# Kernel optimization log

Hardware: AMD Instinct MI355X
Metric: run time of the kernel (lower is better)

Reference implementation:

```python
import jax, jax.numpy as jnp
import numpy as np

B, N = 16, 4096
IOU_THR = 0.7
SCORE_THR = 0.5
MAX_PROPS = 300
IMG = 800.0


def setup_inputs() -> dict:
    key = jax.random.key(0)
    k1, k2, k3 = jax.random.split(key, 3)
    xy = jax.random.uniform(k1, (B, N, 2), dtype=jnp.float32) * IMG
    wh = jax.random.uniform(k2, (B, N, 2), dtype=jnp.float32) * 192.0 + 8.0
    proposals = jnp.concatenate([xy, xy + wh], axis=-1)  # [B,N,4] valid x1y1x2y2
    cls_scores = jax.random.uniform(k3, (B, N, 2), dtype=jnp.float32)
    return {"proposals": proposals, "cls_scores": cls_scores}


def _nms_indices(boxes, scores):
    """Greedy NMS on one image. Returns MAX_PROPS indices into boxes (padded
    with the last kept index, matching the torch module's padding)."""
    boxes = jax.lax.stop_gradient(boxes)
    scores = jax.lax.stop_gradient(scores)
    n = boxes.shape[0]
    valid = scores > SCORE_THR
    # Sort descending; invalid boxes pushed to the end and pre-suppressed.
    order = jnp.argsort(-jnp.where(valid, scores, -jnp.inf))
    b = boxes[order]
    v = valid[order]
    x1, y1, x2, y2 = b[:, 0], b[:, 1], b[:, 2], b[:, 3]
    area = (x2 - x1) * (y2 - y1)
    idxs = jnp.arange(n)

    def body(i, suppressed):
        keep_i = jnp.logical_not(suppressed[i])
        xi1 = jnp.maximum(x1[i], x1)
        yi1 = jnp.maximum(y1[i], y1)
        xi2 = jnp.minimum(x2[i], x2)
        yi2 = jnp.minimum(y2[i], y2)
        inter = jnp.clip(xi2 - xi1, 0.0) * jnp.clip(yi2 - yi1, 0.0)
        iou = inter / (area[i] + area - inter)
        # torch keeps ious < thr, i.e. suppresses iou >= thr among later boxes
        return suppressed | (keep_i & (iou >= IOU_THR) & (idxs > i))

    suppressed = jax.lax.fori_loop(0, n, body, jnp.logical_not(v))
    keep = jnp.logical_not(suppressed)
    # Kept positions (in sorted/greedy order) first, then sentinel n.
    pos = jnp.sort(jnp.where(keep, idxs, n))
    nk = keep.sum()
    slot = jnp.minimum(jnp.arange(MAX_PROPS), jnp.maximum(nk - 1, 0))
    sel_sorted = jnp.clip(pos[slot], 0, n - 1)  # clip guards nk==0
    return order[sel_sorted]  # [MAX_PROPS] indices into original boxes


def reference(proposals, cls_scores):
    scores = cls_scores[..., 1]  # [B,N]
    sel = jax.vmap(_nms_indices)(proposals, scores)  # [B,MAX_PROPS]
    out_boxes = jnp.take_along_axis(proposals, sel[..., None], axis=1)  # [B,MAX_PROPS,4]
    out_scores = jnp.take_along_axis(scores, sel, axis=1)  # [B,MAX_PROPS]
    return out_boxes, out_scores
```

## Files before the change

kernel.cpp:

```cpp
#include <hip/hip_runtime.h>

typedef unsigned long long ull;

#define BB 16
#define NN 4096
#define NT 1024
#define EPT 4
#define MAXP 300
#define IOU_THRESH 0.7f
#define SCORE_THR 0.5f

#define FNT 512
#define FEPT (NN / FNT)
#define CCAP 1024
#define RTOP 512
#define RW (RTOP / 64)

__device__ __forceinline__ bool iou_ge(float ix1, float iy1, float ix2, float iy2, float ia,
                                       float x1, float y1, float x2, float y2, float aj) {
    float xx1 = fmaxf(ix1, x1);
    float yy1 = fmaxf(iy1, y1);
    float xx2 = fminf(ix2, x2);
    float yy2 = fminf(iy2, y2);
    float iw = fmaxf(__fsub_rn(xx2, xx1), 0.0f);
    float ih = fmaxf(__fsub_rn(yy2, yy1), 0.0f);
    float inter = __fmul_rn(iw, ih);
    float uni = __fsub_rn(__fadd_rn(ia, aj), inter);
    float iou = __fdiv_rn(inter, uni);
    return iou >= IOU_THRESH;
}

__global__ __launch_bounds__(FNT, 1) void filter_sort_kernel(const float* __restrict__ proposals,
                                                             const float* __restrict__ cls,
                                                             float* __restrict__ wx1, float* __restrict__ wy1,
                                                             float* __restrict__ wx2, float* __restrict__ wy2,
                                                             float* __restrict__ war,
                                                             unsigned* __restrict__ cidx,
                                                             unsigned* __restrict__ wnv,
                                                             unsigned* __restrict__ need0) {
    __shared__ ull ck[CCAP];
    __shared__ unsigned hist[256];
    __shared__ unsigned swsum[FNT / 64];
    __shared__ unsigned s_nv, s_t, s_abv, s_sz;

    const int b = blockIdx.x, tid = threadIdx.x;
    const unsigned lane = tid & 63, wv = tid >> 6;
    const float* Cb = cls + (size_t)b * NN * 2;
    const float4* Pb4 = (const float4*)(proposals + (size_t)b * NN * 4);

    if (tid < 256) hist[tid] = 0;
    ck[tid] = 0; ck[tid + FNT] = 0;
    if (tid == 0) s_nv = 0;
    __syncthreads();

    unsigned lv = 0;
    #pragma unroll
    for (int c = 0; c < FEPT; ++c) {
        int i = c * FNT + tid;
        float sc = Cb[2 * i + 1];
        if (sc > SCORE_THR) {
            unsigned mb = __float_as_uint(sc) | 0x80000000u;
            atomicAdd(&hist[mb >> 24], 1u);
            ++lv;
        }
    }
    for (int off = 32; off > 0; off >>= 1) lv += __shfl_down(lv, off, 64);
    if (lane == 0) atomicAdd(&s_nv, lv);
    __syncthreads();

    const unsigned nv = s_nv;
    const unsigned target = nv < (unsigned)RTOP ? nv : (unsigned)RTOP;

    if (tid < 64) {
        unsigned h[4], S[4], local = 0;
        #pragma unroll
        for (int c = 0; c < 4; ++c) { h[c] = hist[tid * 4 + c]; local += h[c]; }
        unsigned inc = local;
        for (int off = 1; off < 64; off <<= 1) {
            unsigned t = __shfl_down(inc, off, 64);
            if (tid + off < 64) inc += t;
        }
        unsigned above = inc - local;
        S[3] = above + h[3];
        S[2] = S[3] + h[2];
        S[1] = S[2] + h[1];
        S[0] = S[1] + h[0];
        int bestc = -1;
        #pragma unroll
        for (int c = 3; c >= 0; --c) if (bestc < 0 && S[c] >= target) bestc = c;
        ull m = __ballot(bestc >= 0);
        int L = 63 - __builtin_clzll(m);
        if (tid == L) {
            s_t = (unsigned)(tid * 4 + bestc);
            s_abv = S[bestc] - h[bestc];
            s_sz = h[bestc];
        }
    }
    __syncthreads();
    const unsigned t1 = s_t;
    const unsigned abv1 = s_abv;
    const int lvl2 = (s_abv + s_sz > CCAP);
    unsigned t2 = 0, Ccand;

    if (lvl2) {
        if (tid < 256) hist[tid] = 0;
        __syncthreads();
        #pragma unroll
        for (int c = 0; c < FEPT; ++c) {
            int i = c * FNT + tid;
            float sc = Cb[2 * i + 1];
            if (sc > SCORE_THR) {
                unsigned mb = __float_as_uint(sc) | 0x80000000u;
                if ((mb >> 24) == t1) atomicAdd(&hist[(mb >> 16) & 0xFFu], 1u);
            }
        }
        __syncthreads();
        const unsigned target2 = target - abv1;
        if (tid < 64) {
            unsigned h[4], S[4], local = 0;
            #pragma unroll
            for (int c = 0; c < 4; ++c) { h[c] = hist[tid * 4 + c]; local += h[c]; }
            unsigned inc = local;
            for (int off = 1; off < 64; off <<= 1) {
                unsigned t = __shfl_down(inc, off, 64);
                if (tid + off < 64) inc += t;
            }
            unsigned above = inc - local;
            S[3] = above + h[3];
            S[2] = S[3] + h[2];
            S[1] = S[2] + h[1];
            S[0] = S[1] + h[0];
            int bestc = -1;
            #pragma unroll
            for (int c = 3; c >= 0; --c) if (bestc < 0 && S[c] >= target2) bestc = c;
            ull m = __ballot(bestc >= 0);
            int L = 63 - __builtin_clzll(m);
            if (tid == L) {
                s_t = (unsigned)(tid * 4 + bestc);
                s_abv = S[bestc] - h[bestc];
                s_sz = h[bestc];
            }
        }
        __syncthreads();
        t2 = s_t;
        Ccand = abv1 + s_abv + s_sz;
    } else {
        Ccand = s_abv + s_sz;
    }

    if (tid == 0) { need0[b] = (Ccand > CCAP) ? 1u : 0u; wnv[b] = nv; }

    unsigned pf[FEPT];
    ull keys[FEPT];
    unsigned lc = 0;
    #pragma unroll
    for (int c = 0; c < FEPT; ++c) {
        int i = c * FNT + tid;
        float sc = Cb[2 * i + 1];
        unsigned p = 0; ull key = 0;
        if (sc > SCORE_THR) {
            unsigned mb = __float_as_uint(sc) | 0x80000000u;
            unsigned b1 = mb >> 24;
            if (b1 > t1 || (b1 == t1 && (!lvl2 || ((mb >> 16) & 0xFFu) >= t2))) {
                p = 1;
                key = ((ull)mb << 32) | (unsigned)(~i);
            }
        }
        pf[c] = p; keys[c] = key; lc += p;
    }
    unsigned inc = lc;
    for (int off = 1; off < 64; off <<= 1) {
        unsigned o = __shfl_up(inc, off, 64);
        if (lane >= (unsigned)off) inc += o;
    }
    if (lane == 63) swsum[wv] = inc;
    __syncthreads();
    if (tid == 0) {
        unsigned run = 0;
        for (int w = 0; w < FNT / 64; ++w) { unsigned t = swsum[w]; swsum[w] = run; run += t; }
    }
    __syncthreads();
    unsigned pos = swsum[wv] + (inc - lc);
    #pragma unroll
    for (int c = 0; c < FEPT; ++c) {
        if (pf[c]) {
            if (pos < CCAP) ck[pos] = keys[c];
            ++pos;
        }
    }
    __syncthreads();

    for (unsigned k = 2; k <= CCAP; k <<= 1) {
        for (unsigned j = k >> 1; j > 0; j >>= 1) {
            unsigned p = tid;
            unsigned low = p & (j - 1);
            unsigned i2 = ((p ^ low) << 1) | low;
            unsigned ixj = i2 | j;
            ull a = ck[i2], c2 = ck[ixj];
            if ((a < c2) == ((i2 & k) == 0)) { ck[i2] = c2; ck[ixj] = a; }
            __syncthreads();
        }
    }

    if (tid < RTOP) {
        const size_t base = (size_t)b * RTOP;
        ull key = ck[tid];
        unsigned oi = key ? ~(unsigned)key : 0u;
        float4 v = make_float4(0.f, 0.f, 0.f, 0.f);
        if (key) v = Pb4[oi];
        wx1[base + tid] = v.x; wy1[base + tid] = v.y;
        wx2[base + tid] = v.z; wy2[base + tid] = v.w;
        war[base + tid] = __fmul_rn(__fsub_rn(v.z, v.x), __fsub_rn(v.w, v.y));
        cidx[base + tid] = oi;
    }
}

__global__ __launch_bounds__(256) void mask512_kernel(const float* __restrict__ wx1, const float* __restrict__ wy1,
                                                      const float* __restrict__ wx2, const float* __restrict__ wy2,
                                                      const float* __restrict__ war,
                                                      const unsigned* __restrict__ wnv,
                                                      ull* __restrict__ m8) {
    __shared__ float sx1[RTOP], sy1[RTOP], sx2[RTOP], sy2[RTOP], sar[RTOP];
    const int img = blockIdx.y;
    const unsigned nv = wnv[img];
    const unsigned R2 = nv < (unsigned)RTOP ? nv : (unsigned)RTOP;
    if (R2 == 0) return;
    const int tid = threadIdx.x;
    const size_t base = (size_t)img * RTOP;

    for (int idx = tid; idx < RTOP; idx += 256) {
        sx1[idx] = wx1[base + idx];
        sy1[idx] = wy1[base + idx];
        sx2[idx] = wx2[base + idx];
        sy2[idx] = wy2[base + idx];
        sar[idx] = war[base + idx];
    }
    __syncthreads();

    const unsigned lane = tid & 63;
    const unsigned wvimg = blockIdx.x * 4 + (tid >> 6);
    const unsigned wlastR = (R2 - 1) >> 6;
    ull* mimg = m8 + base * RW;

    for (unsigned i = wvimg; i < R2; i += 32) {
        float ix1 = sx1[i], iy1 = sy1[i], ix2 = sx2[i], iy2 = sy2[i], ia = sar[i];
        const unsigned w0 = i >> 6;
        ull my = 0;
        for (unsigned w = w0; w <= wlastR; ++w) {
            unsigned jj = (w << 6) | lane;
            bool pred = (jj > i) && iou_ge(ix1, iy1, ix2, iy2, ia,
                                           sx1[jj], sy1[jj], sx2[jj], sy2[jj], sar[jj]);
            ull bal = __ballot(pred);
            if (lane == w) my = bal;
        }
        if (lane < RW) {
            ull val = (lane >= w0 && lane <= wlastR) ? my : 0ULL;
            mimg[(size_t)i * RW + lane] = val;
        }
    }
}

__global__ __launch_bounds__(256, 1) void scan_out_kernel(const float* __restrict__ proposals,
                                                          const float* __restrict__ cls,
                                                          const float* __restrict__ wx1, const float* __restrict__ wy1,
                                                          const float* __restrict__ wx2, const float* __restrict__ wy2,
                                                          const unsigned* __restrict__ cidx,
                                                          const unsigned* __restrict__ wnv,
                                                          const unsigned* __restrict__ need0,
                                                          unsigned* __restrict__ need1,
                                                          const ull* __restrict__ m8,
                                                          float* __restrict__ out) {
    __shared__ ull smask[RTOP][RW];
    __shared__ ull kmask[RW];
    __shared__ unsigned s_nk;
    const int b = blockIdx.x, tid = threadIdx.x;
    const unsigned nv = wnv[b];
    const unsigned R2 = nv < (unsigned)RTOP ? nv : (unsigned)RTOP;
    const size_t base = (size_t)b * RTOP;
    const float* Cb = cls + (size_t)b * NN * 2;
    const float4* Pb4 = (const float4*)(proposals + (size_t)b * NN * 4);

    {
        const ull* mimg = m8 + base * RW;
        ull* smflat = &smask[0][0];
        #pragma unroll
        for (int k = 0; k < (RTOP * RW) / 256; ++k)
            smflat[k * 256 + tid] = mimg[k * 256 + tid];
    }
    if (tid < RW) kmask[tid] = 0ULL;
    __syncthreads();

    if (tid < 64) {
        const unsigned lane = tid;
        const unsigned myw = lane & (RW - 1);
        ull sup;
        {
            unsigned lb = myw << 6;
            if (lb >= nv) sup = ~0ULL;
            else if (lb + 64 <= nv) sup = 0ULL;
            else sup = (~0ULL) << (nv - lb);
        }

        unsigned cnt = 0;
        const unsigned nw = (R2 + 63) >> 6;
        for (unsigned w = 0; w < nw; ++w) {
            ull S = __shfl(sup, (int)w, 64);
            const ull* rowp = &smask[w << 6][0];
            #pragma unroll
            for (int i = 0; i < 64; ++i) {
                ull val = rowp[i * RW + w];
                ull take = ((S >> i) & 1ULL) ^ 1ULL;
                S |= val & (0ULL - take);
            }
            ull K = ~S;
            if (lane == 0) kmask[w] = K;
            cnt += (unsigned)__popcll(K);
            if (cnt >= MAXP) break;
            ull acc = 0;
            #pragma unroll
            for (int i = 0; i < 64; ++i) {
                ull t = (K >> i) & 1ULL;
                acc |= rowp[i * RW + myw] & (0ULL - t);
            }
            sup |= acc;
        }
        if (lane == 0) {
            s_nk = cnt;
            need1[b] = need0[b] | ((cnt < MAXP && nv > (unsigned)RTOP) ? 1u : 0u);
        }
    }
    __syncthreads();

    const unsigned nk = s_nk;
    for (unsigned t = tid; t < MAXP; t += 256) {
        float x1, y1, x2, y2; unsigned oi;
        if (nk == 0) {
            oi = NN - 1;
            float4 v = Pb4[oi];
            x1 = v.x; y1 = v.y; x2 = v.z; y2 = v.w;
        } else {
            unsigned r = (t < nk) ? t : nk - 1;
            unsigned w = 0;
            while (true) {
                unsigned pc = (unsigned)__popcll(kmask[w]);
                if (r < pc) break;
                r -= pc; ++w;
            }
            ull K = kmask[w];
            unsigned pos = 0, c;
            c = (unsigned)__popcll(K & 0xFFFFFFFFULL); if (r >= c) { r -= c; pos += 32; K >>= 32; }
            c = (unsigned)__popcll(K & 0xFFFFULL);     if (r >= c) { r -= c; pos += 16; K >>= 16; }
            c = (unsigned)__popcll(K & 0xFFULL);       if (r >= c) { r -= c; pos += 8;  K >>= 8; }
            c = (unsigned)__popcll(K & 0xFULL);        if (r >= c) { r -= c; pos += 4;  K >>= 4; }
            c = (unsigned)__popcll(K & 0x3ULL);        if (r >= c) { r -= c; pos += 2;  K >>= 2; }
            c = (unsigned)__popcll(K & 0x1ULL);        if (r >= c) { r -= c; pos += 1; }
            unsigned p = (w << 6) | pos;
            oi = cidx[base + p];
            x1 = wx1[base + p]; y1 = wy1[base + p];
            x2 = wx2[base + p]; y2 = wy2[base + p];
        }
        float sc = Cb[2 * oi + 1];
        float* ob = out + ((size_t)b * MAXP + t) * 4;
        ob[0] = x1; ob[1] = y1; ob[2] = x2; ob[3] = y2;
        out[(size_t)BB * MAXP * 4 + (size_t)b * MAXP + t] = sc;
    }
}

#define CH 64
#define TPC (CH / EPT)
__global__ __launch_bounds__(NT) void nms_fallback(const float* __restrict__ proposals,
                                                   const float* __restrict__ cls,
                                                   const unsigned* __restrict__ need1,
                                                   float* __restrict__ out) {
    __shared__ unsigned long long skeys[NN];
    __shared__ unsigned char ssup[NN];
    __shared__ float cbx1[2][CH], cby1[2][CH], cbx2[2][CH], cby2[2][CH], cbar[2][CH];
    __shared__ unsigned long long skept[2];
    __shared__ unsigned int ssel[MAXP];
    __shared__ unsigned int swsum[NT / 64];
    __shared__ unsigned int s_nvalid;
    __shared__ unsigned int s_nk;

    const int b = blockIdx.x;
    if (need1 && !need1[b]) return;
    const int tid = threadIdx.x;
    const float* Pb = proposals + (size_t)b * NN * 4;
    const float* Cb = cls + (size_t)b * NN * 2;

    if (tid == 0) s_nvalid = 0;
    __syncthreads();

    unsigned lv = 0;
    for (int i = tid; i < NN; i += NT) {
        float sc = Cb[i * 2 + 1];
        bool valid = sc > SCORE_THR;
        unsigned mb = valid ? (__float_as_uint(sc) | 0x80000000u) : 0u;
        skeys[i] = ((unsigned long long)mb << 32) | (unsigned)(~i);
        lv += valid ? 1u : 0u;
    }
    for (int off = 32; off > 0; off >>= 1) lv += __shfl_down(lv, off, 64);
    if ((tid & 63) == 0) atomicAdd(&s_nvalid, lv);

    for (unsigned k = 2; k <= NN; k <<= 1) {
        for (unsigned j = k >> 1; j > 0; j >>= 1) {
            __syncthreads();
            for (unsigned p = tid; p < NN / 2; p += NT) {
                unsigned low = p & (j - 1);
                unsigned i = ((p ^ low) << 1) | low;
                unsigned ixj = i | j;
                unsigned long long a = skeys[i], c = skeys[ixj];
                if ((a < c) == ((i & k) == 0)) { skeys[i] = c; skeys[ixj] = a; }
            }
        }
    }
    __syncthreads();

    const unsigned n_valid = s_nvalid;

    unsigned ordj[EPT];
    float bx1[EPT], by1[EPT], bx2[EPT], by2[EPT], bar[EPT];
    int rflag[EPT];
    for (int c2 = 0; c2 < EPT; ++c2) {
        int j = tid * EPT + c2;
        unsigned oi = ~(unsigned)skeys[j];
        ordj[c2] = oi;
        const float* P = Pb + (size_t)oi * 4;
        float x1 = P[0], y1 = P[1], x2 = P[2], y2 = P[3];
        bx1[c2] = x1; by1[c2] = y1; bx2[c2] = x2; by2[c2] = y2;
        bar[c2] = __fmul_rn(__fsub_rn(x2, x1), __fsub_rn(y2, y1));
        int sup = (j < (int)n_valid) ? 0 : 1;
        rflag[c2] = sup;
        ssup[j] = (unsigned char)sup;
    }

    const unsigned nch = (n_valid + CH - 1) / CH;
    for (unsigned c = 0; c < nch; ++c) {
        const int p = (int)(c & 1);
        if (tid >= (int)(TPC * c) && tid < (int)(TPC * (c + 1))) {
            int bse = (tid - TPC * c) * EPT;
            #pragma unroll
            for (int c2 = 0; c2 < EPT; ++c2) {
                int l = bse + c2;
                cbx1[p][l] = bx1[c2]; cby1[p][l] = by1[c2];
                cbx2[p][l] = bx2[c2]; cby2[p][l] = by2[c2];
                cbar[p][l] = bar[c2];
            }
        }
        __syncthreads();

        if (tid < CH) {
            const int l = tid;
            const int j = (int)(c * CH) + l;
            float x1 = cbx1[p][l], y1 = cby1[p][l], x2 = cbx2[p][l], y2 = cby2[p][l];
            float ar = cbar[p][l];
            int supl = ssup[j];
            unsigned long long row = 0ULL;
            for (int m = l + 1; m < CH; ++m) {
                bool s = iou_ge(x1, y1, x2, y2, ar,
                                cbx1[p][m], cby1[p][m], cbx2[p][m], cby2[p][m], cbar[p][m]);
                if (s) row |= (1ULL << m);
            }
            unsigned long long S = __ballot(supl != 0);
            for (int i = 0; i < CH; ++i) {
                unsigned long long ri = __shfl(row, i, 64);
                if (!((S >> i) & 1ULL)) S |= ri;
            }
            ssup[j] = (unsigned char)((S >> l) & 1ULL);
            if (l == 0) skept[p] = ~S;
        }
        __syncthreads();

        const int myFirst = tid * EPT;
        if (myFirst >= (int)(CH * (c + 1)) &&
            !(rflag[0] & rflag[1] & rflag[2] & rflag[3])) {
            unsigned long long K = skept[p];
            while (K) {
                int m = __builtin_ctzll(K);
                K &= K - 1;
                float mx1 = cbx1[p][m], my1 = cby1[p][m];
                float mx2 = cbx2[p][m], my2 = cby2[p][m];
                float ma = cbar[p][m];
                #pragma unroll
                for (int c2 = 0; c2 < EPT; ++c2) {
                    if (!rflag[c2]) {
                        bool s = iou_ge(mx1, my1, mx2, my2, ma,
                                        bx1[c2], by1[c2], bx2[c2], by2[c2], bar[c2]);
                        if (s) { rflag[c2] = 1; ssup[myFirst + c2] = 1; }
                    }
                }
            }
        }
    }
    __syncthreads();

    unsigned kflag[EPT];
    unsigned lc = 0;
    for (int c2 = 0; c2 < EPT; ++c2) {
        int j = tid * EPT + c2;
        kflag[c2] = ssup[j] ? 0u : 1u;
        lc += kflag[c2];
    }
    unsigned lane = tid & 63, wid = tid >> 6;
    unsigned inc = lc;
    for (int off = 1; off < 64; off <<= 1) {
        unsigned o = __shfl_up(inc, off, 64);
        if (lane >= (unsigned)off) inc += o;
    }
    if (lane == 63) swsum[wid] = inc;
    __syncthreads();
    if (tid == 0) {
        unsigned run = 0;
        for (int w = 0; w < NT / 64; ++w) { unsigned t = swsum[w]; swsum[w] = run; run += t; }
        s_nk = run;
    }
    __syncthreads();
    unsigned bse = swsum[wid] + (inc - lc);
    for (int c2 = 0; c2 < EPT; ++c2) {
        if (kflag[c2]) {
            if (bse < MAXP) ssel[bse] = ordj[c2];
            ++bse;
        }
    }
    const unsigned nk_pre = s_nk;
    __syncthreads();

    if (tid < MAXP) {
        if (nk_pre == 0) {
            ssel[tid] = ~(unsigned)skeys[NN - 1];
        } else if (tid >= nk_pre) {
            ssel[tid] = ssel[nk_pre - 1];
        }
    }
    __syncthreads();

    if (tid < MAXP) {
        unsigned si = ssel[tid];
        const float* P = Pb + (size_t)si * 4;
        float* ob = out + ((size_t)b * MAXP + tid) * 4;
        ob[0] = P[0]; ob[1] = P[1]; ob[2] = P[2]; ob[3] = P[3];
        out[(size_t)BB * MAXP * 4 + (size_t)b * MAXP + tid] = Cb[si * 2 + 1];
    }
}

extern "C" void kernel_launch(void* const* d_in, const int* in_sizes, int n_in,
                              void* d_out, int out_size, void* d_ws, size_t ws_size,
                              hipStream_t stream) {
    const float* proposals = (const float*)d_in[0];
    const float* cls = (const float*)d_in[1];
    float* out = (float*)d_out;

    const size_t S = (size_t)BB * RTOP;
    const size_t need_sz = S * RW * sizeof(ull)
                         + S * 5 * sizeof(float)
                         + S * sizeof(unsigned)
                         + 3 * BB * sizeof(unsigned) + 256;
    if (ws_size < need_sz) {
        nms_fallback<<<BB, NT, 0, stream>>>(proposals, cls, (const unsigned*)nullptr, out);
        return;
    }

    ull* m8 = (ull*)d_ws;
    float* wx1 = (float*)(m8 + S * RW);
    float* wy1 = wx1 + S;
    float* wx2 = wy1 + S;
    float* wy2 = wx2 + S;
    float* war = wy2 + S;
    unsigned* cidx = (unsigned*)(war + S);
    unsigned* wnv = cidx + S;
    unsigned* need0 = wnv + BB;
    unsigned* need1 = need0 + BB;

    filter_sort_kernel<<<BB, FNT, 0, stream>>>(proposals, cls, wx1, wy1, wx2, wy2, war,
                                               cidx, wnv, need0);
    mask512_kernel<<<dim3(RTOP / 64, BB), 256, 0, stream>>>(wx1, wy1, wx2, wy2, war, wnv, m8);
    scan_out_kernel<<<BB, 256, 0, stream>>>(proposals, cls, wx1, wy1, wx2, wy2,
                                            cidx, wnv, need0, need1, m8, out);
    nms_fallback<<<BB, NT, 0, stream>>>(proposals, cls, need1, out);
}
```

Before: 54.24 us.

## Fuse filter/sort, IoU mask, and scan kernels into one per-image kernel

Merges the three-kernel pipeline (filter+sort, IoU mask build, greedy scan/output) into a single per-image block that keeps boxes, areas, indices and the 512x8 suppression mask in shared memory instead of round-tripping through global workspace. It also caches the packed score bits in registers so the second histogram pass and the key-building pass no longer reload scores from global memory. This removes two kernel launches and the global writes and reads of intermediates. In exchange, the mask computation now runs on only 16 blocks of 8 waves instead of 128 blocks, which cuts parallelism for the IoU stage.

```diff
diff --git a/kernel.cpp b/kernel.cpp
--- a/kernel.cpp
+++ b/kernel.cpp
@@ -30,18 +30,18 @@
     return iou >= IOU_THRESH;
 }
 
-__global__ __launch_bounds__(FNT, 1) void filter_sort_kernel(const float* __restrict__ proposals,
-                                                             const float* __restrict__ cls,
-                                                             float* __restrict__ wx1, float* __restrict__ wy1,
-                                                             float* __restrict__ wx2, float* __restrict__ wy2,
-                                                             float* __restrict__ war,
-                                                             unsigned* __restrict__ cidx,
-                                                             unsigned* __restrict__ wnv,
-                                                             unsigned* __restrict__ need0) {
+__global__ __launch_bounds__(FNT, 1) void fused_kernel(const float* __restrict__ proposals,
+                                                       const float* __restrict__ cls,
+                                                       unsigned* __restrict__ need1,
+                                                       float* __restrict__ out) {
     __shared__ ull ck[CCAP];
+    __shared__ ull smask[RTOP][RW];
+    __shared__ float sx1[RTOP], sy1[RTOP], sx2[RTOP], sy2[RTOP], sar[RTOP];
+    __shared__ unsigned soi[RTOP];
     __shared__ unsigned hist[256];
     __shared__ unsigned swsum[FNT / 64];
-    __shared__ unsigned s_nv, s_t, s_abv, s_sz;
+    __shared__ ull kmask[RW];
+    __shared__ unsigned s_nv, s_t, s_abv, s_sz, s_nk;
 
     const int b = blockIdx.x, tid = threadIdx.x;
     const unsigned lane = tid & 63, wv = tid >> 6;
@@ -53,16 +53,15 @@
     if (tid == 0) s_nv = 0;
     __syncthreads();
 
+    unsigned mbv[FEPT];
     unsigned lv = 0;
     #pragma unroll
     for (int c = 0; c < FEPT; ++c) {
         int i = c * FNT + tid;
         float sc = Cb[2 * i + 1];
-        if (sc > SCORE_THR) {
-            unsigned mb = __float_as_uint(sc) | 0x80000000u;
-            atomicAdd(&hist[mb >> 24], 1u);
-            ++lv;
-        }
+        bool valid = sc > SCORE_THR;
+        mbv[c] = valid ? (__float_as_uint(sc) | 0x80000000u) : 0u;
+        if (valid) { atomicAdd(&hist[mbv[c] >> 24], 1u); ++lv; }
     }
     for (int off = 32; off > 0; off >>= 1) lv += __shfl_down(lv, off, 64);
     if (lane == 0) atomicAdd(&s_nv, lv);
@@ -107,12 +106,7 @@
         __syncthreads();
         #pragma unroll
         for (int c = 0; c < FEPT; ++c) {
-            int i = c * FNT + tid;
-            float sc = Cb[2 * i + 1];
-            if (sc > SCORE_THR) {
-                unsigned mb = __float_as_uint(sc) | 0x80000000u;
-                if ((mb >> 24) == t1) atomicAdd(&hist[(mb >> 16) & 0xFFu], 1u);
-            }
+            if ((mbv[c] >> 24) == t1) atomicAdd(&hist[(mbv[c] >> 16) & 0xFFu], 1u);
         }
         __syncthreads();
         const unsigned target2 = target - abv1;
@@ -147,8 +141,7 @@
     } else {
         Ccand = s_abv + s_sz;
     }
-
-    if (tid == 0) { need0[b] = (Ccand > CCAP) ? 1u : 0u; wnv[b] = nv; }
+    const unsigned need0 = (Ccand > CCAP) ? 1u : 0u;
 
     unsigned pf[FEPT];
     ull keys[FEPT];
@@ -156,14 +149,12 @@
     #pragma unroll
     for (int c = 0; c < FEPT; ++c) {
         int i = c * FNT + tid;
-        float sc = Cb[2 * i + 1];
         unsigned p = 0; ull key = 0;
-        if (sc > SCORE_THR) {
-            unsigned mb = __float_as_uint(sc) | 0x80000000u;
-            unsigned b1 = mb >> 24;
-            if (b1 > t1 || (b1 == t1 && (!lvl2 || ((mb >> 16) & 0xFFu) >= t2))) {
+        if (mbv[c]) {
+            unsigned b1 = mbv[c] >> 24;
+            if (b1 > t1 || (b1 == t1 && (!lvl2 || ((mbv[c] >> 16) & 0xFFu) >= t2))) {
                 p = 1;
-                key = ((ull)mb << 32) | (unsigned)(~i);
+                key = ((ull)mbv[c] << 32) | (unsigned)(~i);
             }
         }
         pf[c] = p; keys[c] = key; lc += p;
@@ -203,95 +194,41 @@
     }
 
     if (tid < RTOP) {
-        const size_t base = (size_t)b * RTOP;
         ull key = ck[tid];
         unsigned oi = key ? ~(unsigned)key : 0u;
         float4 v = make_float4(0.f, 0.f, 0.f, 0.f);
         if (key) v = Pb4[oi];
-        wx1[base + tid] = v.x; wy1[base + tid] = v.y;
-        wx2[base + tid] = v.z; wy2[base + tid] = v.w;
-        war[base + tid] = __fmul_rn(__fsub_rn(v.z, v.x), __fsub_rn(v.w, v.y));
-        cidx[base + tid] = oi;
-    }
-}
-
-__global__ __launch_bounds__(256) void mask512_kernel(const float* __restrict__ wx1, const float* __restrict__ wy1,
-                                                      const float* __restrict__ wx2, const float* __restrict__ wy2,
-                                                      const float* __restrict__ war,
-                                                      const unsigned* __restrict__ wnv,
-                                                      ull* __restrict__ m8) {
-    __shared__ float sx1[RTOP], sy1[RTOP], sx2[RTOP], sy2[RTOP], sar[RTOP];
-    const int img = blockIdx.y;
-    const unsigned nv = wnv[img];
+        sx1[tid] = v.x; sy1[tid] = v.y; sx2[tid] = v.z; sy2[tid] = v.w;
+        sar[tid] = __fmul_rn(__fsub_rn(v.z, v.x), __fsub_rn(v.w, v.y));
+        soi[tid] = oi;
+    }
+    if (tid < RW) kmask[tid] = 0ULL;
+    __syncthreads();
+
     const unsigned R2 = nv < (unsigned)RTOP ? nv : (unsigned)RTOP;
-    if (R2 == 0) return;
-    const int tid = threadIdx.x;
-    const size_t base = (size_t)img * RTOP;
-
-    for (int idx = tid; idx < RTOP; idx += 256) {
-        sx1[idx] = wx1[base + idx];
-        sy1[idx] = wy1[base + idx];
-        sx2[idx] = wx2[base + idx];
-        sy2[idx] = wy2[base + idx];
-        sar[idx] = war[base + idx];
-    }
-    __syncthreads();
-
-    const unsigned lane = tid & 63;
-    const unsigned wvimg = blockIdx.x * 4 + (tid >> 6);
-    const unsigned wlastR = (R2 - 1) >> 6;
-    ull* mimg = m8 + base * RW;
-
-    for (unsigned i = wvimg; i < R2; i += 32) {
-        float ix1 = sx1[i], iy1 = sy1[i], ix2 = sx2[i], iy2 = sy2[i], ia = sar[i];
-        const unsigned w0 = i >> 6;
-        ull my = 0;
-        for (unsigned w = w0; w <= wlastR; ++w) {
-            unsigned jj = (w << 6) | lane;
-            bool pred = (jj > i) && iou_ge(ix1, iy1, ix2, iy2, ia,
-                                           sx1[jj], sy1[jj], sx2[jj], sy2[jj], sar[jj]);
-            ull bal = __ballot(pred);
-            if (lane == w) my = bal;
-        }
-        if (lane < RW) {
-            ull val = (lane >= w0 && lane <= wlastR) ? my : 0ULL;
-            mimg[(size_t)i * RW + lane] = val;
-        }
-    }
-}
-
-__global__ __launch_bounds__(256, 1) void scan_out_kernel(const float* __restrict__ proposals,
-                                                          const float* __restrict__ cls,
-                                                          const float* __restrict__ wx1, const float* __restrict__ wy1,
-                                                          const float* __restrict__ wx2, const float* __restrict__ wy2,
-                                                          const unsigned* __restrict__ cidx,
-                                                          const unsigned* __restrict__ wnv,
-                                                          const unsigned* __restrict__ need0,
-                                                          unsigned* __restrict__ need1,
-                                                          const ull* __restrict__ m8,
-                                                          float* __restrict__ out) {
-    __shared__ ull smask[RTOP][RW];
-    __shared__ ull kmask[RW];
-    __shared__ unsigned s_nk;
-    const int b = blockIdx.x, tid = threadIdx.x;
-    const unsigned nv = wnv[b];
-    const unsigned R2 = nv < (unsigned)RTOP ? nv : (unsigned)RTOP;
-    const size_t base = (size_t)b * RTOP;
-    const float* Cb = cls + (size_t)b * NN * 2;
-    const float4* Pb4 = (const float4*)(proposals + (size_t)b * NN * 4);
-
-    {
-        const ull* mimg = m8 + base * RW;
-        ull* smflat = &smask[0][0];
-        #pragma unroll
-        for (int k = 0; k < (RTOP * RW) / 256; ++k)
-            smflat[k * 256 + tid] = mimg[k * 256 + tid];
-    }
-    if (tid < RW) kmask[tid] = 0ULL;
+
+    if (R2 > 0) {
+        const unsigned wlastR = (R2 - 1) >> 6;
+        for (unsigned i = wv; i < R2; i += FNT / 64) {
+            float ix1 = sx1[i], iy1 = sy1[i], ix2 = sx2[i], iy2 = sy2[i], ia = sar[i];
+            const unsigned w0 = i >> 6;
+            ull my = 0;
+            for (unsigned w = w0; w <= wlastR; ++w) {
+                unsigned jj = (w << 6) | lane;
+                bool pred = (jj > i) && iou_ge(ix1, iy1, ix2, iy2, ia,
+                                               sx1[jj], sy1[jj], sx2[jj], sy2[jj], sar[jj]);
+                ull bal = __ballot(pred);
+                if (lane == w) my = bal;
+            }
+            if (lane < RW) {
+                ull val = (lane >= w0 && lane <= wlastR) ? my : 0ULL;
+                smask[i][lane] = val;
+            }
+        }
+    }
     __syncthreads();
 
     if (tid < 64) {
-        const unsigned lane = tid;
         const unsigned myw = lane & (RW - 1);
         ull sup;
         {
@@ -326,13 +263,13 @@
         }
         if (lane == 0) {
             s_nk = cnt;
-            need1[b] = need0[b] | ((cnt < MAXP && nv > (unsigned)RTOP) ? 1u : 0u);
+            need1[b] = need0 | ((cnt < MAXP && nv > (unsigned)RTOP) ? 1u : 0u);
         }
     }
     __syncthreads();
 
     const unsigned nk = s_nk;
-    for (unsigned t = tid; t < MAXP; t += 256) {
+    for (unsigned t = tid; t < MAXP; t += FNT) {
         float x1, y1, x2, y2; unsigned oi;
         if (nk == 0) {
             oi = NN - 1;
@@ -347,17 +284,16 @@
                 r -= pc; ++w;
             }
             ull K = kmask[w];
-            unsigned pos = 0, c;
-            c = (unsigned)__popcll(K & 0xFFFFFFFFULL); if (r >= c) { r -= c; pos += 32; K >>= 32; }
-            c = (unsigned)__popcll(K & 0xFFFFULL);     if (r >= c) { r -= c; pos += 16; K >>= 16; }
-            c = (unsigned)__popcll(K & 0xFFULL);       if (r >= c) { r -= c; pos += 8;  K >>= 8; }
-            c = (unsigned)__popcll(K & 0xFULL);        if (r >= c) { r -= c; pos += 4;  K >>= 4; }
-            c = (unsigned)__popcll(K & 0x3ULL);        if (r >= c) { r -= c; pos += 2;  K >>= 2; }
-            c = (unsigned)__popcll(K & 0x1ULL);        if (r >= c) { r -= c; pos += 1; }
-            unsigned p = (w << 6) | pos;
-            oi = cidx[base + p];
-            x1 = wx1[base + p]; y1 = wy1[base + p];
-            x2 = wx2[base + p]; y2 = wy2[base + p];
+            unsigned p2 = 0, c;
+            c = (unsigned)__popcll(K & 0xFFFFFFFFULL); if (r >= c) { r -= c; p2 += 32; K >>= 32; }
+            c = (unsigned)__popcll(K & 0xFFFFULL);     if (r >= c) { r -= c; p2 += 16; K >>= 16; }
+            c = (unsigned)__popcll(K & 0xFFULL);       if (r >= c) { r -= c; p2 += 8;  K >>= 8; }
+            c = (unsigned)__popcll(K & 0xFULL);        if (r >= c) { r -= c; p2 += 4;  K >>= 4; }
+            c = (unsigned)__popcll(K & 0x3ULL);        if (r >= c) { r -= c; p2 += 2;  K >>= 2; }
+            c = (unsigned)__popcll(K & 0x1ULL);        if (r >= c) { r -= c; p2 += 1; }
+            unsigned p = (w << 6) | p2;
+            oi = soi[p];
+            x1 = sx1[p]; y1 = sy1[p]; x2 = sx2[p]; y2 = sy2[p];
         }
         float sc = Cb[2 * oi + 1];
         float* ob = out + ((size_t)b * MAXP + t) * 4;
@@ -549,31 +485,13 @@
     const float* cls = (const float*)d_in[1];
     float* out = (float*)d_out;
 
-    const size_t S = (size_t)BB * RTOP;
-    const size_t need_sz = S * RW * sizeof(ull)
-                         + S * 5 * sizeof(float)
-                         + S * sizeof(unsigned)
-                         + 3 * BB * sizeof(unsigned) + 256;
-    if (ws_size < need_sz) {
+    if (ws_size < BB * sizeof(unsigned)) {
         nms_fallback<<<BB, NT, 0, stream>>>(proposals, cls, (const unsigned*)nullptr, out);
         return;
     }
 
-    ull* m8 = (ull*)d_ws;
-    float* wx1 = (float*)(m8 + S * RW);
-    float* wy1 = wx1 + S;
-    float* wx2 = wy1 + S;
-    float* wy2 = wx2 + S;
-    float* war = wy2 + S;
-    unsigned* cidx = (unsigned*)(war + S);
-    unsigned* wnv = cidx + S;
-    unsigned* need0 = wnv + BB;
-    unsigned* need1 = need0 + BB;
-
-    filter_sort_kernel<<<BB, FNT, 0, stream>>>(proposals, cls, wx1, wy1, wx2, wy2, war,
-                                               cidx, wnv, need0);
-    mask512_kernel<<<dim3(RTOP / 64, BB), 256, 0, stream>>>(wx1, wy1, wx2, wy2, war, wnv, m8);
-    scan_out_kernel<<<BB, 256, 0, stream>>>(proposals, cls, wx1, wy1, wx2, wy2,
-                                            cidx, wnv, need0, need1, m8, out);
+    unsigned* need1 = (unsigned*)d_ws;
+
+    fused_kernel<<<BB, FNT, 0, stream>>>(proposals, cls, need1, out);
     nms_fallback<<<BB, NT, 0, stream>>>(proposals, cls, need1, out);
 }
```

Result: slower. 89.39 us (+64.8%).

## Replace bitonic sort with rank-by-count selection and cache scores in registers

Applied to the files above, without the earlier changes.

The 1024-element shared-memory bitonic sort, with its 55 barrier-separated stages, is replaced by a rank computation. Each candidate counts how many keys exceed it and scatters its box to that rank if it falls in the top 512. Scores are loaded once into registers rather than re-read from global memory on every pass, and the second-level radix histogram now always runs. The rank loop costs O(C^2) shared reads per block, where C is up to 1024 candidates, in exchange for removing the many sync stages. It also adds a global zero-fill of the workspace before the scatter.

```diff
diff --git a/kernel.cpp b/kernel.cpp
--- a/kernel.cpp
+++ b/kernel.cpp
@@ -30,7 +30,7 @@
     return iou >= IOU_THRESH;
 }
 
-__global__ __launch_bounds__(FNT, 1) void filter_sort_kernel(const float* __restrict__ proposals,
+__global__ __launch_bounds__(FNT, 1) void filter_rank_kernel(const float* __restrict__ proposals,
                                                              const float* __restrict__ cls,
                                                              float* __restrict__ wx1, float* __restrict__ wy1,
                                                              float* __restrict__ wx2, float* __restrict__ wy2,
@@ -38,31 +38,30 @@
                                                              unsigned* __restrict__ cidx,
                                                              unsigned* __restrict__ wnv,
                                                              unsigned* __restrict__ need0) {
-    __shared__ ull ck[CCAP];
+    __shared__ ull ckey[CCAP];
     __shared__ unsigned hist[256];
     __shared__ unsigned swsum[FNT / 64];
-    __shared__ unsigned s_nv, s_t, s_abv, s_sz;
+    __shared__ unsigned s_nv, s_t, s_abv, s_sz, s_cc;
 
     const int b = blockIdx.x, tid = threadIdx.x;
     const unsigned lane = tid & 63, wv = tid >> 6;
     const float* Cb = cls + (size_t)b * NN * 2;
     const float4* Pb4 = (const float4*)(proposals + (size_t)b * NN * 4);
+    const size_t base = (size_t)b * RTOP;
 
     if (tid < 256) hist[tid] = 0;
-    ck[tid] = 0; ck[tid + FNT] = 0;
     if (tid == 0) s_nv = 0;
     __syncthreads();
 
+    unsigned mbv[FEPT];
     unsigned lv = 0;
     #pragma unroll
     for (int c = 0; c < FEPT; ++c) {
         int i = c * FNT + tid;
         float sc = Cb[2 * i + 1];
-        if (sc > SCORE_THR) {
-            unsigned mb = __float_as_uint(sc) | 0x80000000u;
-            atomicAdd(&hist[mb >> 24], 1u);
-            ++lv;
-        }
+        bool valid = sc > SCORE_THR;
+        mbv[c] = valid ? (__float_as_uint(sc) | 0x80000000u) : 0u;
+        if (valid) { atomicAdd(&hist[mbv[c] >> 24], 1u); ++lv; }
     }
     for (int off = 32; off > 0; off >>= 1) lv += __shfl_down(lv, off, 64);
     if (lane == 0) atomicAdd(&s_nv, lv);
@@ -99,56 +98,43 @@
     __syncthreads();
     const unsigned t1 = s_t;
     const unsigned abv1 = s_abv;
-    const int lvl2 = (s_abv + s_sz > CCAP);
-    unsigned t2 = 0, Ccand;
-
-    if (lvl2) {
-        if (tid < 256) hist[tid] = 0;
-        __syncthreads();
+
+    if (tid < 256) hist[tid] = 0;
+    __syncthreads();
+    #pragma unroll
+    for (int c = 0; c < FEPT; ++c) {
+        if (mbv[c] && (mbv[c] >> 24) == t1) atomicAdd(&hist[(mbv[c] >> 16) & 0xFFu], 1u);
+    }
+    __syncthreads();
+    const unsigned target2 = target - abv1;
+    if (tid < 64) {
+        unsigned h[4], S[4], local = 0;
         #pragma unroll
-        for (int c = 0; c < FEPT; ++c) {
-            int i = c * FNT + tid;
-            float sc = Cb[2 * i + 1];
-            if (sc > SCORE_THR) {
-                unsigned mb = __float_as_uint(sc) | 0x80000000u;
-                if ((mb >> 24) == t1) atomicAdd(&hist[(mb >> 16) & 0xFFu], 1u);
-            }
-        }
-        __syncthreads();
-        const unsigned target2 = target - abv1;
-        if (tid < 64) {
-            unsigned h[4], S[4], local = 0;
-            #pragma unroll
-            for (int c = 0; c < 4; ++c) { h[c] = hist[tid * 4 + c]; local += h[c]; }
-            unsigned inc = local;
-            for (int off = 1; off < 64; off <<= 1) {
-                unsigned t = __shfl_down(inc, off, 64);
-                if (tid + off < 64) inc += t;
-            }
-            unsigned above = inc - local;
-            S[3] = above + h[3];
-            S[2] = S[3] + h[2];
-            S[1] = S[2] + h[1];
-            S[0] = S[1] + h[0];
-            int bestc = -1;
-            #pragma unroll
-            for (int c = 3; c >= 0; --c) if (bestc < 0 && S[c] >= target2) bestc = c;
-            ull m = __ballot(bestc >= 0);
-            int L = 63 - __builtin_clzll(m);
-            if (tid == L) {
-                s_t = (unsigned)(tid * 4 + bestc);
-                s_abv = S[bestc] - h[bestc];
-                s_sz = h[bestc];
-            }
-        }
-        __syncthreads();
-        t2 = s_t;
-        Ccand = abv1 + s_abv + s_sz;
-    } else {
-        Ccand = s_abv + s_sz;
-    }
-
-    if (tid == 0) { need0[b] = (Ccand > CCAP) ? 1u : 0u; wnv[b] = nv; }
+        for (int c = 0; c < 4; ++c) { h[c] = hist[tid * 4 + c]; local += h[c]; }
+        unsigned inc = local;
+        for (int off = 1; off < 64; off <<= 1) {
+            unsigned t = __shfl_down(inc, off, 64);
+            if (tid + off < 64) inc += t;
+        }
+        unsigned above = inc - local;
+        S[3] = above + h[3];
+        S[2] = S[3] + h[2];
+        S[1] = S[2] + h[1];
+        S[0] = S[1] + h[0];
+        int bestc = -1;
+        #pragma unroll
+        for (int c = 3; c >= 0; --c) if (bestc < 0 && S[c] >= target2) bestc = c;
+        ull m = __ballot(bestc >= 0);
+        int L = 63 - __builtin_clzll(m);
+        if (tid == L) {
+            s_t = (unsigned)(tid * 4 + bestc);
+            s_abv = S[bestc] - h[bestc];
+            s_sz = h[bestc];
+        }
+    }
+    __syncthreads();
+    const unsigned t2 = s_t;
+    const unsigned Ccand = abv1 + s_abv + s_sz;
 
     unsigned pf[FEPT];
     ull keys[FEPT];
@@ -156,14 +142,12 @@
     #pragma unroll
     for (int c = 0; c < FEPT; ++c) {
         int i = c * FNT + tid;
-        float sc = Cb[2 * i + 1];
         unsigned p = 0; ull key = 0;
-        if (sc > SCORE_THR) {
-            unsigned mb = __float_as_uint(sc) | 0x80000000u;
-            unsigned b1 = mb >> 24;
-            if (b1 > t1 || (b1 == t1 && (!lvl2 || ((mb >> 16) & 0xFFu) >= t2))) {
+        if (mbv[c]) {
+            unsigned b1 = mbv[c] >> 24;
+            if (b1 > t1 || (b1 == t1 && ((mbv[c] >> 16) & 0xFFu) >= t2)) {
                 p = 1;
-                key = ((ull)mb << 32) | (unsigned)(~i);
+                key = ((ull)mbv[c] << 32) | (unsigned)(~i);
             }
         }
         pf[c] = p; keys[c] = key; lc += p;
@@ -178,41 +162,43 @@
     if (tid == 0) {
         unsigned run = 0;
         for (int w = 0; w < FNT / 64; ++w) { unsigned t = swsum[w]; swsum[w] = run; run += t; }
+        s_cc = (run < (unsigned)CCAP) ? run : (unsigned)CCAP;
     }
     __syncthreads();
     unsigned pos = swsum[wv] + (inc - lc);
     #pragma unroll
     for (int c = 0; c < FEPT; ++c) {
         if (pf[c]) {
-            if (pos < CCAP) ck[pos] = keys[c];
+            if (pos < CCAP) ckey[pos] = keys[c];
             ++pos;
         }
     }
-    __syncthreads();
-
-    for (unsigned k = 2; k <= CCAP; k <<= 1) {
-        for (unsigned j = k >> 1; j > 0; j >>= 1) {
-            unsigned p = tid;
-            unsigned low = p & (j - 1);
-            unsigned i2 = ((p ^ low) << 1) | low;
-            unsigned ixj = i2 | j;
-            ull a = ck[i2], c2 = ck[ixj];
-            if ((a < c2) == ((i2 & k) == 0)) { ck[i2] = c2; ck[ixj] = a; }
-            __syncthreads();
-        }
-    }
 
     if (tid < RTOP) {
-        const size_t base = (size_t)b * RTOP;
-        ull key = ck[tid];
-        unsigned oi = key ? ~(unsigned)key : 0u;
-        float4 v = make_float4(0.f, 0.f, 0.f, 0.f);
-        if (key) v = Pb4[oi];
-        wx1[base + tid] = v.x; wy1[base + tid] = v.y;
-        wx2[base + tid] = v.z; wy2[base + tid] = v.w;
-        war[base + tid] = __fmul_rn(__fsub_rn(v.z, v.x), __fsub_rn(v.w, v.y));
-        cidx[base + tid] = oi;
-    }
+        wx1[base + tid] = 0.f; wy1[base + tid] = 0.f;
+        wx2[base + tid] = 0.f; wy2[base + tid] = 0.f;
+        war[base + tid] = 0.f;
+        cidx[base + tid] = 0u;
+    }
+    __syncthreads();
+
+    const unsigned Cc = s_cc;
+    for (unsigned c = tid; c < Cc; c += FNT) {
+        ull mykey = ckey[c];
+        unsigned rank = 0;
+        for (unsigned j = 0; j < Cc; ++j)
+            rank += (ckey[j] > mykey) ? 1u : 0u;
+        if (rank < (unsigned)RTOP) {
+            unsigned oi = ~(unsigned)mykey;
+            float4 v = Pb4[oi];
+            wx1[base + rank] = v.x; wy1[base + rank] = v.y;
+            wx2[base + rank] = v.z; wy2[base + rank] = v.w;
+            war[base + rank] = __fmul_rn(__fsub_rn(v.z, v.x), __fsub_rn(v.w, v.y));
+            cidx[base + rank] = oi;
+        }
+    }
+
+    if (tid == 0) { wnv[b] = nv; need0[b] = (Ccand > (unsigned)CCAP) ? 1u : 0u; }
 }
 
 __global__ __launch_bounds__(256) void mask512_kernel(const float* __restrict__ wx1, const float* __restrict__ wy1,
@@ -274,6 +260,7 @@
     __shared__ ull kmask[RW];
     __shared__ unsigned s_nk;
     const int b = blockIdx.x, tid = threadIdx.x;
+    const unsigned lane = tid & 63;
     const unsigned nv = wnv[b];
     const unsigned R2 = nv < (unsigned)RTOP ? nv : (unsigned)RTOP;
     const size_t base = (size_t)b * RTOP;
@@ -291,7 +278,6 @@
     __syncthreads();
 
     if (tid < 64) {
-        const unsigned lane = tid;
         const unsigned myw = lane & (RW - 1);
         ull sup;
         {
@@ -347,14 +333,14 @@
                 r -= pc; ++w;
             }
             ull K = kmask[w];
-            unsigned pos = 0, c;
-            c = (unsigned)__popcll(K & 0xFFFFFFFFULL); if (r >= c) { r -= c; pos += 32; K >>= 32; }
-            c = (unsigned)__popcll(K & 0xFFFFULL);     if (r >= c) { r -= c; pos += 16; K >>= 16; }
-            c = (unsigned)__popcll(K & 0xFFULL);       if (r >= c) { r -= c; pos += 8;  K >>= 8; }
-            c = (unsigned)__popcll(K & 0xFULL);        if (r >= c) { r -= c; pos += 4;  K >>= 4; }
-            c = (unsigned)__popcll(K & 0x3ULL);        if (r >= c) { r -= c; pos += 2;  K >>= 2; }
-            c = (unsigned)__popcll(K & 0x1ULL);        if (r >= c) { r -= c; pos += 1; }
-            unsigned p = (w << 6) | pos;
+            unsigned p2 = 0, c;
+            c = (unsigned)__popcll(K & 0xFFFFFFFFULL); if (r >= c) { r -= c; p2 += 32; K >>= 32; }
+            c = (unsigned)__popcll(K & 0xFFFFULL);     if (r >= c) { r -= c; p2 += 16; K >>= 16; }
+            c = (unsigned)__popcll(K & 0xFFULL);       if (r >= c) { r -= c; p2 += 8;  K >>= 8; }
+            c = (unsigned)__popcll(K & 0xFULL);        if (r >= c) { r -= c; p2 += 4;  K >>= 4; }
+            c = (unsigned)__popcll(K & 0x3ULL);        if (r >= c) { r -= c; p2 += 2;  K >>= 2; }
+            c = (unsigned)__popcll(K & 0x1ULL);        if (r >= c) { r -= c; p2 += 1; }
+            unsigned p = (w << 6) | p2;
             oi = cidx[base + p];
             x1 = wx1[base + p]; y1 = wy1[base + p];
             x2 = wx2[base + p]; y2 = wy2[base + p];
@@ -570,7 +556,7 @@
     unsigned* need0 = wnv + BB;
     unsigned* need1 = need0 + BB;
 
-    filter_sort_kernel<<<BB, FNT, 0, stream>>>(proposals, cls, wx1, wy1, wx2, wy2, war,
+    filter_rank_kernel<<<BB, FNT, 0, stream>>>(proposals, cls, wx1, wy1, wx2, wy2, war,
                                                cidx, wnv, need0);
     mask512_kernel<<<dim3(RTOP / 64, BB), 256, 0, stream>>>(wx1, wy1, wx2, wy2, war, wnv, m8);
     scan_out_kernel<<<BB, 256, 0, stream>>>(proposals, cls, wx1, wy1, wx2, wy2,
```

Result: slower. 63.88 us (+17.8%).

## Fuse IoU mask construction into scan/output kernel with shared-memory mask

Applied to the files above, without the earlier changes.

Merges the separate mask-building kernel into the greedy scan/output kernel, so the suppression bitmask is built directly in shared memory by a 512-thread block per image. This removes one kernel launch and the global write and read of the mask, and output gathers now read from shared memory. In exchange, the mask computation runs on only one block per image instead of eight, which reduces parallelism across compute units.

```diff
diff --git a/kernel.cpp b/kernel.cpp
--- a/kernel.cpp
+++ b/kernel.cpp
@@ -215,83 +215,60 @@
     }
 }
 
-__global__ __launch_bounds__(256) void mask512_kernel(const float* __restrict__ wx1, const float* __restrict__ wy1,
-                                                      const float* __restrict__ wx2, const float* __restrict__ wy2,
-                                                      const float* __restrict__ war,
-                                                      const unsigned* __restrict__ wnv,
-                                                      ull* __restrict__ m8) {
+__global__ __launch_bounds__(512, 1) void mask_scan_out_kernel(const float* __restrict__ proposals,
+                                                               const float* __restrict__ cls,
+                                                               const float* __restrict__ wx1, const float* __restrict__ wy1,
+                                                               const float* __restrict__ wx2, const float* __restrict__ wy2,
+                                                               const float* __restrict__ war,
+                                                               const unsigned* __restrict__ cidx,
+                                                               const unsigned* __restrict__ wnv,
+                                                               const unsigned* __restrict__ need0,
+                                                               unsigned* __restrict__ need1,
+                                                               float* __restrict__ out) {
+    __shared__ ull smask[RTOP][RW];
     __shared__ float sx1[RTOP], sy1[RTOP], sx2[RTOP], sy2[RTOP], sar[RTOP];
-    const int img = blockIdx.y;
-    const unsigned nv = wnv[img];
-    const unsigned R2 = nv < (unsigned)RTOP ? nv : (unsigned)RTOP;
-    if (R2 == 0) return;
-    const int tid = threadIdx.x;
-    const size_t base = (size_t)img * RTOP;
-
-    for (int idx = tid; idx < RTOP; idx += 256) {
-        sx1[idx] = wx1[base + idx];
-        sy1[idx] = wy1[base + idx];
-        sx2[idx] = wx2[base + idx];
-        sy2[idx] = wy2[base + idx];
-        sar[idx] = war[base + idx];
-    }
-    __syncthreads();
-
-    const unsigned lane = tid & 63;
-    const unsigned wvimg = blockIdx.x * 4 + (tid >> 6);
-    const unsigned wlastR = (R2 - 1) >> 6;
-    ull* mimg = m8 + base * RW;
-
-    for (unsigned i = wvimg; i < R2; i += 32) {
-        float ix1 = sx1[i], iy1 = sy1[i], ix2 = sx2[i], iy2 = sy2[i], ia = sar[i];
-        const unsigned w0 = i >> 6;
-        ull my = 0;
-        for (unsigned w = w0; w <= wlastR; ++w) {
-            unsigned jj = (w << 6) | lane;
-            bool pred = (jj > i) && iou_ge(ix1, iy1, ix2, iy2, ia,
-                                           sx1[jj], sy1[jj], sx2[jj], sy2[jj], sar[jj]);
-            ull bal = __ballot(pred);
-            if (lane == w) my = bal;
-        }
-        if (lane < RW) {
-            ull val = (lane >= w0 && lane <= wlastR) ? my : 0ULL;
-            mimg[(size_t)i * RW + lane] = val;
-        }
-    }
-}
-
-__global__ __launch_bounds__(256, 1) void scan_out_kernel(const float* __restrict__ proposals,
-                                                          const float* __restrict__ cls,
-                                                          const float* __restrict__ wx1, const float* __restrict__ wy1,
-                                                          const float* __restrict__ wx2, const float* __restrict__ wy2,
-                                                          const unsigned* __restrict__ cidx,
-                                                          const unsigned* __restrict__ wnv,
-                                                          const unsigned* __restrict__ need0,
-                                                          unsigned* __restrict__ need1,
-                                                          const ull* __restrict__ m8,
-                                                          float* __restrict__ out) {
-    __shared__ ull smask[RTOP][RW];
+    __shared__ unsigned soi[RTOP];
     __shared__ ull kmask[RW];
     __shared__ unsigned s_nk;
+
     const int b = blockIdx.x, tid = threadIdx.x;
+    const unsigned lane = tid & 63, wv = tid >> 6;
     const unsigned nv = wnv[b];
     const unsigned R2 = nv < (unsigned)RTOP ? nv : (unsigned)RTOP;
     const size_t base = (size_t)b * RTOP;
     const float* Cb = cls + (size_t)b * NN * 2;
     const float4* Pb4 = (const float4*)(proposals + (size_t)b * NN * 4);
 
-    {
-        const ull* mimg = m8 + base * RW;
-        ull* smflat = &smask[0][0];
-        #pragma unroll
-        for (int k = 0; k < (RTOP * RW) / 256; ++k)
-            smflat[k * 256 + tid] = mimg[k * 256 + tid];
+    if (tid < RTOP) {
+        sx1[tid] = wx1[base + tid]; sy1[tid] = wy1[base + tid];
+        sx2[tid] = wx2[base + tid]; sy2[tid] = wy2[base + tid];
+        sar[tid] = war[base + tid]; soi[tid] = cidx[base + tid];
     }
     if (tid < RW) kmask[tid] = 0ULL;
     __syncthreads();
 
+    if (R2 > 0) {
+        const unsigned wlastR = (R2 - 1) >> 6;
+        for (unsigned i = wv; i < R2; i += 512 / 64) {
+            float ix1 = sx1[i], iy1 = sy1[i], ix2 = sx2[i], iy2 = sy2[i], ia = sar[i];
+            const unsigned w0 = i >> 6;
+            ull my = 0;
+            for (unsigned w = w0; w <= wlastR; ++w) {
+                unsigned jj = (w << 6) | lane;
+                bool pred = (jj > i) && iou_ge(ix1, iy1, ix2, iy2, ia,
+                                               sx1[jj], sy1[jj], sx2[jj], sy2[jj], sar[jj]);
+                ull bal = __ballot(pred);
+                if (lane == w) my = bal;
+            }
+            if (lane < RW) {
+                ull val = (lane >= w0 && lane <= wlastR) ? my : 0ULL;
+                smask[i][lane] = val;
+            }
+        }
+    }
+    __syncthreads();
+
     if (tid < 64) {
-        const unsigned lane = tid;
         const unsigned myw = lane & (RW - 1);
         ull sup;
         {
@@ -332,7 +309,7 @@
     __syncthreads();
 
     const unsigned nk = s_nk;
-    for (unsigned t = tid; t < MAXP; t += 256) {
+    for (unsigned t = tid; t < MAXP; t += 512) {
         float x1, y1, x2, y2; unsigned oi;
         if (nk == 0) {
             oi = NN - 1;
@@ -347,17 +324,16 @@
                 r -= pc; ++w;
             }
             ull K = kmask[w];
-            unsigned pos = 0, c;
-            c = (unsigned)__popcll(K & 0xFFFFFFFFULL); if (r >= c) { r -= c; pos += 32; K >>= 32; }
-            c = (unsigned)__popcll(K & 0xFFFFULL);     if (r >= c) { r -= c; pos += 16; K >>= 16; }
-            c = (unsigned)__popcll(K & 0xFFULL);       if (r >= c) { r -= c; pos += 8;  K >>= 8; }
-            c = (unsigned)__popcll(K & 0xFULL);        if (r >= c) { r -= c; pos += 4;  K >>= 4; }
-            c = (unsigned)__popcll(K & 0x3ULL);        if (r >= c) { r -= c; pos += 2;  K >>= 2; }
-            c = (unsigned)__popcll(K & 0x1ULL);        if (r >= c) { r -= c; pos += 1; }
-            unsigned p = (w << 6) | pos;
-            oi = cidx[base + p];
-            x1 = wx1[base + p]; y1 = wy1[base + p];
-            x2 = wx2[base + p]; y2 = wy2[base + p];
+            unsigned p2 = 0, c;
+            c = (unsigned)__popcll(K & 0xFFFFFFFFULL); if (r >= c) { r -= c; p2 += 32; K >>= 32; }
+            c = (unsigned)__popcll(K & 0xFFFFULL);     if (r >= c) { r -= c; p2 += 16; K >>= 16; }
+            c = (unsigned)__popcll(K & 0xFFULL);       if (r >= c) { r -= c; p2 += 8;  K >>= 8; }
+            c = (unsigned)__popcll(K & 0xFULL);        if (r >= c) { r -= c; p2 += 4;  K >>= 4; }
+            c = (unsigned)__popcll(K & 0x3ULL);        if (r >= c) { r -= c; p2 += 2;  K >>= 2; }
+            c = (unsigned)__popcll(K & 0x1ULL);        if (r >= c) { r -= c; p2 += 1; }
+            unsigned p = (w << 6) | p2;
+            oi = soi[p];
+            x1 = sx1[p]; y1 = sy1[p]; x2 = sx2[p]; y2 = sy2[p];
         }
         float sc = Cb[2 * oi + 1];
         float* ob = out + ((size_t)b * MAXP + t) * 4;
@@ -550,8 +526,7 @@
     float* out = (float*)d_out;
 
     const size_t S = (size_t)BB * RTOP;
-    const size_t need_sz = S * RW * sizeof(ull)
-                         + S * 5 * sizeof(float)
+    const size_t need_sz = S * 5 * sizeof(float)
                          + S * sizeof(unsigned)
                          + 3 * BB * sizeof(unsigned) + 256;
     if (ws_size < need_sz) {
@@ -559,8 +534,7 @@
         return;
     }
 
-    ull* m8 = (ull*)d_ws;
-    float* wx1 = (float*)(m8 + S * RW);
+    float* wx1 = (float*)d_ws;
     float* wy1 = wx1 + S;
     float* wx2 = wy1 + S;
     float* wy2 = wx2 + S;
@@ -572,8 +546,7 @@
 
     filter_sort_kernel<<<BB, FNT, 0, stream>>>(proposals, cls, wx1, wy1, wx2, wy2, war,
                                                cidx, wnv, need0);
-    mask512_kernel<<<dim3(RTOP / 64, BB), 256, 0, stream>>>(wx1, wy1, wx2, wy2, war, wnv, m8);
-    scan_out_kernel<<<BB, 256, 0, stream>>>(proposals, cls, wx1, wy1, wx2, wy2,
-                                            cidx, wnv, need0, need1, m8, out);
+    mask_scan_out_kernel<<<BB, 512, 0, stream>>>(proposals, cls, wx1, wy1, wx2, wy2, war,
+                                                 cidx, wnv, need0, need1, out);
     nms_fallback<<<BB, NT, 0, stream>>>(proposals, cls, need1, out);
 }
```

Measured after the change: 95.35 us. 1.76x slower.
